# Performance work log

Hardware: AMD Instinct MI355X
Metric: run time of the kernel (lower is better)

## Reference

```python
import jax, jax.numpy as jnp
import numpy as np

B, D, H, T = 2048, 16, 256, 50
BETA_MIN, BETA_MAX = 0.1, 20.0


def setup_inputs() -> dict:
    key = jax.random.key(0)
    ks = jax.random.split(key, 6)
    s1 = 1.0 / np.sqrt(D)
    s2 = 1.0 / np.sqrt(H)
    return {
        "x": jax.random.normal(ks[0], (B, D), dtype=jnp.float32),
        "W1": jax.random.normal(ks[1], (D, H), dtype=jnp.float32) * s1,
        "b1": jnp.zeros((H,), dtype=jnp.float32),
        "wt": jax.random.normal(ks[2], (H,), dtype=jnp.float32) * 0.1,
        "W2": jax.random.normal(ks[3], (H, D), dtype=jnp.float32) * s2,
        "b2": jnp.zeros((D,), dtype=jnp.float32),
    }


def _dynamics(x, t, W1, b1, wt, W2, b2):
    # Reverse-time probability-flow ODE drift for a VP-SDE:
    #   dx/dt = f(x,t) - 0.5 * g(t)^2 * score(x,t)
    # with f = -0.5*beta(t)*x, g^2 = beta(t), score = MLP(x, t).
    beta = BETA_MIN + t * (BETA_MAX - BETA_MIN)
    h = jnp.tanh(x @ W1 + t * wt + b1)  # [B, H]
    score = h @ W2 + b2                 # [B, D]
    return -0.5 * beta * (x + score)


def _trace_jac(f, x):
    # Exact per-sample trace of the [D, D] Jacobian of f (batched over B)
    # via D forward-mode JVPs with basis tangents (batched, no per-output loop).
    eye = jnp.eye(x.shape[-1], dtype=x.dtype)

    def jvp_col(e):
        _, jv = jax.jvp(f, (x,), (jnp.broadcast_to(e, x.shape),))
        return jv  # [B, D]

    cols = jax.vmap(jvp_col)(eye)       # [D, B, D]
    return jnp.einsum("ibi->b", cols)   # sum of Jacobian diagonal per sample


def reference(x, W1, b1, wt, W2, b2):
    times = jnp.linspace(1e-3, 1.0, T, dtype=jnp.float32)

    def F(xc, t):
        dyn = lambda y: _dynamics(y, t, W1, b1, wt, W2, b2)
        dx = dyn(xc)
        tr = _trace_jac(dyn, xc)
        return dx, tr

    def rk4_step(carry, ts):
        xc, ldj = carry
        t0, t1 = ts
        h = t1 - t0
        k1x, k1t = F(xc, t0)
        k2x, k2t = F(xc + 0.5 * h * k1x, t0 + 0.5 * h)
        k3x, k3t = F(xc + 0.5 * h * k2x, t0 + 0.5 * h)
        k4x, k4t = F(xc + h * k3x, t1)
        xn = xc + (h / 6.0) * (k1x + 2.0 * k2x + 2.0 * k3x + k4x)
        ln = ldj + (h / 6.0) * (k1t + 2.0 * k2t + 2.0 * k3t + k4t)
        return (xn, ln), (xn, ln)

    ldj0 = jnp.zeros((x.shape[0],), dtype=x.dtype)
    (xf, ldjf), (xs, _) = jax.lax.scan(
        rk4_step, (x, ldj0), (times[:-1], times[1:])
    )
    xt = jnp.concatenate([x[None], xs], axis=0)  # [T, B, D] trajectory
    return xf, ldjf, xt
```

## Files before the change

### kernel.cpp

```cpp
#include <hip/hip_runtime.h>
#include <stdint.h>


typedef _Float16 f16x2 __attribute__((ext_vector_type(2)));

#if defined(__has_builtin)
#if __has_builtin(__builtin_amdgcn_fdot2)
#define HAVE_FDOT2 1
#endif
#endif

__device__ __forceinline__ float fdot2f(f16x2 a, f16x2 b, float c) {
#ifdef HAVE_FDOT2
    return __builtin_amdgcn_fdot2(a, b, c, false);
#else
    return fmaf((float)a.y, (float)b.y, fmaf((float)a.x, (float)b.x, c));
#endif
}

__device__ __forceinline__ uint32_t pkz(float a, float b) {
    auto v = __builtin_amdgcn_cvt_pkrtz(a, b);
    return __builtin_bit_cast(uint32_t, v);
}
__device__ __forceinline__ f16x2 upk(uint32_t u) {
    return __builtin_bit_cast(f16x2, u);
}

#define DPP_XOR1 0xB1
#define DPP_XOR2 0x4E
#define DPP_RHM  0x141
template <int CTRL>
__device__ __forceinline__ float dpp_add(float x) {
    int v = __builtin_amdgcn_update_dpp(
        0, __builtin_bit_cast(int, x), CTRL, 0xF, 0xF, true);
    return x + __builtin_bit_cast(float, v);
}

#define Bn 2048
#define Dn 16
#define Hn 256
#define Tn 50
#define CH 20

constexpr float T_LO = 1e-3f;
constexpr float DTc  = (1.0f - 1e-3f) / (float)(Tn - 1);
constexpr float W1W  = DTc * (1.f / 6.f);
constexpr float W2W  = DTc * (2.f / 6.f);

constexpr float nh_c(float t) { return -0.5f * (0.1f + 19.9f * t); }
constexpr float wbsum_c() {
    float s = 0.f;
    for (int j = 0; j < Tn - 1; ++j) {
        float t0 = T_LO + (float)j * DTc;
        float tm = t0 + 0.5f * DTc;
        float t1 = t0 + DTc;
        s += W1W * nh_c(t0) + 2.f * W2W * nh_c(tm) + W1W * nh_c(t1);
    }
    return s;
}
constexpr float WBSUM = wbsum_c();

__global__ __launch_bounds__(64) void ode_kernel(
    const float* __restrict__ x_in,
    const float* __restrict__ W1,
    const float* __restrict__ b1v,
    const float* __restrict__ wtv,
    const float* __restrict__ W2,
    const float* __restrict__ b2v,
    float* __restrict__ out)
{
    __shared__ __align__(16) uint32_t h_lds[8 * CH];

    const int L  = threadIdx.x;
    const int g8 = L >> 3;
    const int c  = L & 7;
    const int ia = 2 * g8, ib = ia + 1;
    const int k0 = 4 * L;
    const int gs = blockIdx.x;

    const float K2 = 2.88539008f;

    f16x2 w1p[4][8];
    float b1k[4], wtk[4], ck[4];
    #pragma unroll
    for (int q = 0; q < 4; ++q) {
        const int k = k0 + q;
        #pragma unroll
        for (int j = 0; j < 8; ++j) {
            f16x2 v;
            v.x = (_Float16)(K2 * W1[(2 * j)     * Hn + k]);
            v.y = (_Float16)(K2 * W1[(2 * j + 1) * Hn + k]);
            w1p[q][j] = v;
        }
        b1k[q] = K2 * b1v[k];
        wtk[q] = K2 * wtv[k];
        float s = 0.f;
        #pragma unroll
        for (int ii = 0; ii < 16; ++ii)
            s = fmaf(W1[ii * Hn + k], W2[k * Dn + ii], s);
        ck[q] = s;
    }
    const float cksum = (ck[0] + ck[1]) + (ck[2] + ck[3]);

    f16x2 w2a[16], w2b[16];
    #pragma unroll
    for (int m = 0; m < 16; ++m) {
        f16x2 va, vb;
        va.x = (_Float16)W2[(32 * c + 2 * m)     * Dn + ia];
        va.y = (_Float16)W2[(32 * c + 2 * m + 1) * Dn + ia];
        vb.x = (_Float16)W2[(32 * c + 2 * m)     * Dn + ib];
        vb.y = (_Float16)W2[(32 * c + 2 * m + 1) * Dn + ib];
        w2a[m] = va; w2b[m] = vb;
    }
    const float b2a8 = 0.125f * b2v[ia];
    const float b2b8 = 0.125f * b2v[ib];

    float xa = x_in[gs * Dn + ia];
    float xb = x_in[gs * Dn + ib];
    float ldjl = 0.f;

    float* xf_out  = out;
    float* ldj_out = out + (size_t)Bn * Dn;
    float* xt_ptr  = out + (size_t)Bn * Dn + Bn + gs * Dn + ia;

    if (c == 0) *(float2*)xt_ptr = make_float2(xa, xb);
    xt_ptr += Bn * Dn;

    const int hwidx = CH * (L >> 3) + 2 * (L & 7);

    uint32_t se0, se1, se2, se3, se4, se5, se6, se7;
    auto bcast = [&](float ea, float eb) {
        const uint32_t vpk = pkz(ea, eb);
        se0 = __builtin_amdgcn_readlane(vpk,  0);
        se1 = __builtin_amdgcn_readlane(vpk,  8);
        se2 = __builtin_amdgcn_readlane(vpk, 16);
        se3 = __builtin_amdgcn_readlane(vpk, 24);
        se4 = __builtin_amdgcn_readlane(vpk, 32);
        se5 = __builtin_amdgcn_readlane(vpk, 40);
        se6 = __builtin_amdgcn_readlane(vpk, 48);
        se7 = __builtin_amdgcn_readlane(vpk, 56);
    };

    auto Feval = [&](float xeva, float xevb, const float (&ui)[4],
                     float nhb, float wb, float& dxa, float& dxb) {
        const f16x2 xp[8] = { upk(se0), upk(se1), upk(se2), upk(se3),
                              upk(se4), upk(se5), upk(se6), upk(se7) };
        float u0 = ui[0], u1 = ui[1], u2 = ui[2], u3 = ui[3];
        #pragma unroll
        for (int j = 0; j < 8; ++j) {
            u0 = fdot2f(xp[j], w1p[0][j], u0);
            u1 = fdot2f(xp[j], w1p[1][j], u1);
            u2 = fdot2f(xp[j], w1p[2][j], u2);
            u3 = fdot2f(xp[j], w1p[3][j], u3);
        }
        const float h0 = fmaf(-2.f, __builtin_amdgcn_rcpf(__builtin_amdgcn_exp2f(u0) + 1.f), 1.f);
        const float h1 = fmaf(-2.f, __builtin_amdgcn_rcpf(__builtin_amdgcn_exp2f(u1) + 1.f), 1.f);
        const float h2 = fmaf(-2.f, __builtin_amdgcn_rcpf(__builtin_amdgcn_exp2f(u2) + 1.f), 1.f);
        const float h3 = fmaf(-2.f, __builtin_amdgcn_rcpf(__builtin_amdgcn_exp2f(u3) + 1.f), 1.f);
        *(uint2*)&h_lds[hwidx] = make_uint2(pkz(h0, h1), pkz(h2, h3));

        const float q0 = h0 * h0, q1 = h1 * h1, q2 = h2 * h2, q3 = h3 * h3;
        const float sq = fmaf(q0, ck[0], fmaf(q1, ck[1], fmaf(q2, ck[2], q3 * ck[3])));
        ldjl = fmaf(-wb, sq, ldjl);

        asm volatile("" ::: "memory");

        float sa0 = b2a8, sa1 = 0.f, sb0 = b2b8, sb1 = 0.f;
        #pragma unroll
        for (int mq = 0; mq < 4; ++mq) {
            const uint4 hv = *(const uint4*)&h_lds[CH * c + 4 * mq];
            const f16x2 p0 = upk(hv.x), p1 = upk(hv.y), p2 = upk(hv.z), p3 = upk(hv.w);
            sa0 = fdot2f(p0, w2a[4 * mq + 0], sa0);
            sb0 = fdot2f(p0, w2b[4 * mq + 0], sb0);
            sa1 = fdot2f(p1, w2a[4 * mq + 1], sa1);
            sb1 = fdot2f(p1, w2b[4 * mq + 1], sb1);
            sa0 = fdot2f(p2, w2a[4 * mq + 2], sa0);
            sb0 = fdot2f(p2, w2b[4 * mq + 2], sb0);
            sa1 = fdot2f(p3, w2a[4 * mq + 3], sa1);
            sb1 = fdot2f(p3, w2b[4 * mq + 3], sb1);
        }
        float sca = sa0 + sa1, scb = sb0 + sb1;
        sca = dpp_add<DPP_XOR1>(sca);  scb = dpp_add<DPP_XOR1>(scb);
        sca = dpp_add<DPP_XOR2>(sca);  scb = dpp_add<DPP_XOR2>(scb);
        sca = dpp_add<DPP_RHM >(sca);  scb = dpp_add<DPP_RHM >(scb);

        dxa = nhb * (xeva + sca);
        dxb = nhb * (xevb + scb);
    };

    float ui0[4], uim[4], uit[4];
    #pragma unroll
    for (int q = 0; q < 4; ++q) ui0[q] = fmaf(T_LO, wtk[q], b1k[q]);
    float nhb0 = -0.5f * fmaf(T_LO, 19.9f, 0.1f);

    bcast(xa, xb);
    for (int j = 0; j < Tn - 1; ++j) {
        const float t0 = fmaf((float)j, DTc, T_LO);
        const float tm = t0 + 0.5f * DTc;
        const float t1 = t0 + DTc;
        #pragma unroll
        for (int q = 0; q < 4; ++q) {
            uim[q] = fmaf(tm, wtk[q], b1k[q]);
            uit[q] = fmaf(t1, wtk[q], b1k[q]);
        }
        const float nhbm = -0.5f * fmaf(tm, 19.9f, 0.1f);
        const float nhb1 = -0.5f * fmaf(t1, 19.9f, 0.1f);
        const float wb0 = W1W * nhb0;
        const float wbm = W2W * nhbm;
        const float wb1 = W1W * nhb1;

        float k1a, k1b, k2a, k2b, k3a, k3b, k4a, k4b;

        Feval(xa, xb, ui0, nhb0, wb0, k1a, k1b);
        const float e2a = fmaf(0.5f * DTc, k1a, xa);
        const float e2b = fmaf(0.5f * DTc, k1b, xb);
        bcast(e2a, e2b);
        Feval(e2a, e2b, uim, nhbm, wbm, k2a, k2b);
        const float e3a = fmaf(0.5f * DTc, k2a, xa);
        const float e3b = fmaf(0.5f * DTc, k2b, xb);
        bcast(e3a, e3b);
        Feval(e3a, e3b, uim, nhbm, wbm, k3a, k3b);
        const float e4a = fmaf(DTc, k3a, xa);
        const float e4b = fmaf(DTc, k3b, xb);
        bcast(e4a, e4b);
        Feval(e4a, e4b, uit, nhb1, wb1, k4a, k4b);

        xa = fmaf(W1W, k1a + 2.f * (k2a + k3a) + k4a, xa);
        xb = fmaf(W1W, k1b + 2.f * (k2b + k3b) + k4b, xb);
        if (c == 0) *(float2*)xt_ptr = make_float2(xa, xb);
        xt_ptr += Bn * Dn;
        bcast(xa, xb);

        #pragma unroll
        for (int q = 0; q < 4; ++q) ui0[q] = uit[q];
        nhb0 = nhb1;
    }

    if (c == 0) *(float2*)(xf_out + gs * Dn + ia) = make_float2(xa, xb);

    ldjl = fmaf(cksum + 0.25f, WBSUM, ldjl);
    #pragma unroll
    for (int off = 1; off < 64; off <<= 1)
        ldjl += __shfl_xor(ldjl, off);
    if (L == 0) ldj_out[gs] = ldjl;
}

extern "C" void kernel_launch(void* const* d_in, const int* in_sizes, int n_in,
                              void* d_out, int out_size, void* d_ws, size_t ws_size,
                              hipStream_t stream) {
    const float* x  = (const float*)d_in[0];
    const float* W1 = (const float*)d_in[1];
    const float* b1 = (const float*)d_in[2];
    const float* wt = (const float*)d_in[3];
    const float* W2 = (const float*)d_in[4];
    const float* b2 = (const float*)d_in[5];
    (void)in_sizes; (void)n_in; (void)out_size; (void)d_ws; (void)ws_size;
    ode_kernel<<<Bn, 64, 0, stream>>>(x, W1, b1, wt, W2, b2, (float*)d_out);
}
```

Baseline: 171.9 us.

## Split hidden layer across two wavefronts per sample with double-buffered LDS

Each block now runs 128 threads (two wavefronts) per sample, and each thread handles 2 hidden units instead of 4. This halves the per-wave work in the first layer and the tanh. The second layer is redundantly computed by both waves from a shared, double-buffered LDS buffer of h, which now needs a block barrier on every function evaluation. The log-det partials from the two waves are combined through LDS at the end. The cost is 200 extra __syncthreads per sample, duplicated second-layer work, and more total waves in flight.

```diff
diff --git a/kernel.cpp b/kernel.cpp
--- a/kernel.cpp
+++ b/kernel.cpp
@@ -60,7 +60,7 @@
 }
 constexpr float WBSUM = wbsum_c();
 
-__global__ __launch_bounds__(64) void ode_kernel(
+__global__ __launch_bounds__(128) void ode_kernel(
     const float* __restrict__ x_in,
     const float* __restrict__ W1,
     const float* __restrict__ b1v,
@@ -69,22 +69,23 @@
     const float* __restrict__ b2v,
     float* __restrict__ out)
 {
-    __shared__ __align__(16) uint32_t h_lds[8 * CH];
-
-    const int L  = threadIdx.x;
-    const int g8 = L >> 3;
-    const int c  = L & 7;
+    __shared__ __align__(16) uint32_t h_lds[2][8 * CH];
+    __shared__ float ldj_x[2];
+
+    const int tid = threadIdx.x;
+    const int L   = tid & 63;
+    const int g8  = L >> 3;
+    const int c   = L & 7;
     const int ia = 2 * g8, ib = ia + 1;
-    const int k0 = 4 * L;
     const int gs = blockIdx.x;
 
     const float K2 = 2.88539008f;
 
-    f16x2 w1p[4][8];
-    float b1k[4], wtk[4], ck[4];
-    #pragma unroll
-    for (int q = 0; q < 4; ++q) {
-        const int k = k0 + q;
+    f16x2 w1p[2][8];
+    float b1k[2], wtk[2], ck[2];
+    #pragma unroll
+    for (int q = 0; q < 2; ++q) {
+        const int k = 2 * tid + q;
         #pragma unroll
         for (int j = 0; j < 8; ++j) {
             f16x2 v;
@@ -100,7 +101,7 @@
             s = fmaf(W1[ii * Hn + k], W2[k * Dn + ii], s);
         ck[q] = s;
     }
-    const float cksum = (ck[0] + ck[1]) + (ck[2] + ck[3]);
+    const float cks = ck[0] + ck[1];
 
     f16x2 w2a[16], w2b[16];
     #pragma unroll
@@ -123,10 +124,10 @@
     float* ldj_out = out + (size_t)Bn * Dn;
     float* xt_ptr  = out + (size_t)Bn * Dn + Bn + gs * Dn + ia;
 
-    if (c == 0) *(float2*)xt_ptr = make_float2(xa, xb);
+    if ((tid & 0x47) == 0) *(float2*)xt_ptr = make_float2(xa, xb);
     xt_ptr += Bn * Dn;
 
-    const int hwidx = CH * (L >> 3) + 2 * (L & 7);
+    const int hw = CH * (tid >> 4) + (tid & 15);
 
     uint32_t se0, se1, se2, se3, se4, se5, se6, se7;
     auto bcast = [&](float ea, float eb) {
@@ -141,34 +142,34 @@
         se7 = __builtin_amdgcn_readlane(vpk, 56);
     };
 
-    auto Feval = [&](float xeva, float xevb, const float (&ui)[4],
+    int fe = 0;
+
+    auto Feval = [&](float xeva, float xevb, const float (&ui)[2],
                      float nhb, float wb, float& dxa, float& dxb) {
+        uint32_t* hb = h_lds[fe & 1]; ++fe;
+
         const f16x2 xp[8] = { upk(se0), upk(se1), upk(se2), upk(se3),
                               upk(se4), upk(se5), upk(se6), upk(se7) };
-        float u0 = ui[0], u1 = ui[1], u2 = ui[2], u3 = ui[3];
+        float u0 = ui[0], u1 = ui[1];
         #pragma unroll
         for (int j = 0; j < 8; ++j) {
             u0 = fdot2f(xp[j], w1p[0][j], u0);
             u1 = fdot2f(xp[j], w1p[1][j], u1);
-            u2 = fdot2f(xp[j], w1p[2][j], u2);
-            u3 = fdot2f(xp[j], w1p[3][j], u3);
         }
         const float h0 = fmaf(-2.f, __builtin_amdgcn_rcpf(__builtin_amdgcn_exp2f(u0) + 1.f), 1.f);
         const float h1 = fmaf(-2.f, __builtin_amdgcn_rcpf(__builtin_amdgcn_exp2f(u1) + 1.f), 1.f);
-        const float h2 = fmaf(-2.f, __builtin_amdgcn_rcpf(__builtin_amdgcn_exp2f(u2) + 1.f), 1.f);
-        const float h3 = fmaf(-2.f, __builtin_amdgcn_rcpf(__builtin_amdgcn_exp2f(u3) + 1.f), 1.f);
-        *(uint2*)&h_lds[hwidx] = make_uint2(pkz(h0, h1), pkz(h2, h3));
-
-        const float q0 = h0 * h0, q1 = h1 * h1, q2 = h2 * h2, q3 = h3 * h3;
-        const float sq = fmaf(q0, ck[0], fmaf(q1, ck[1], fmaf(q2, ck[2], q3 * ck[3])));
+        hb[hw] = pkz(h0, h1);
+
+        const float q0 = h0 * h0, q1 = h1 * h1;
+        const float sq = fmaf(q0, ck[0], q1 * ck[1]);
         ldjl = fmaf(-wb, sq, ldjl);
 
-        asm volatile("" ::: "memory");
+        __syncthreads();
 
         float sa0 = b2a8, sa1 = 0.f, sb0 = b2b8, sb1 = 0.f;
         #pragma unroll
         for (int mq = 0; mq < 4; ++mq) {
-            const uint4 hv = *(const uint4*)&h_lds[CH * c + 4 * mq];
+            const uint4 hv = *(const uint4*)&hb[CH * c + 4 * mq];
             const f16x2 p0 = upk(hv.x), p1 = upk(hv.y), p2 = upk(hv.z), p3 = upk(hv.w);
             sa0 = fdot2f(p0, w2a[4 * mq + 0], sa0);
             sb0 = fdot2f(p0, w2b[4 * mq + 0], sb0);
@@ -188,9 +189,9 @@
         dxb = nhb * (xevb + scb);
     };
 
-    float ui0[4], uim[4], uit[4];
-    #pragma unroll
-    for (int q = 0; q < 4; ++q) ui0[q] = fmaf(T_LO, wtk[q], b1k[q]);
+    float ui0[2], uim[2], uit[2];
+    #pragma unroll
+    for (int q = 0; q < 2; ++q) ui0[q] = fmaf(T_LO, wtk[q], b1k[q]);
     float nhb0 = -0.5f * fmaf(T_LO, 19.9f, 0.1f);
 
     bcast(xa, xb);
@@ -199,7 +200,7 @@
         const float tm = t0 + 0.5f * DTc;
         const float t1 = t0 + DTc;
         #pragma unroll
-        for (int q = 0; q < 4; ++q) {
+        for (int q = 0; q < 2; ++q) {
             uim[q] = fmaf(tm, wtk[q], b1k[q]);
             uit[q] = fmaf(t1, wtk[q], b1k[q]);
         }
@@ -227,22 +228,24 @@
 
         xa = fmaf(W1W, k1a + 2.f * (k2a + k3a) + k4a, xa);
         xb = fmaf(W1W, k1b + 2.f * (k2b + k3b) + k4b, xb);
-        if (c == 0) *(float2*)xt_ptr = make_float2(xa, xb);
+        if ((tid & 0x47) == 0) *(float2*)xt_ptr = make_float2(xa, xb);
         xt_ptr += Bn * Dn;
         bcast(xa, xb);
 
         #pragma unroll
-        for (int q = 0; q < 4; ++q) ui0[q] = uit[q];
+        for (int q = 0; q < 2; ++q) ui0[q] = uit[q];
         nhb0 = nhb1;
     }
 
-    if (c == 0) *(float2*)(xf_out + gs * Dn + ia) = make_float2(xa, xb);
-
-    ldjl = fmaf(cksum + 0.25f, WBSUM, ldjl);
+    if ((tid & 0x47) == 0) *(float2*)(xf_out + gs * Dn + ia) = make_float2(xa, xb);
+
+    ldjl = fmaf(cks + 0.125f, WBSUM, ldjl);
     #pragma unroll
     for (int off = 1; off < 64; off <<= 1)
         ldjl += __shfl_xor(ldjl, off);
-    if (L == 0) ldj_out[gs] = ldjl;
+    if (L == 0) ldj_x[tid >> 6] = ldjl;
+    __syncthreads();
+    if (tid == 0) ldj_out[gs] = ldj_x[0] + ldj_x[1];
 }
 
 extern "C" void kernel_launch(void* const* d_in, const int* in_sizes, int n_in,
@@ -255,5 +258,5 @@
     const float* W2 = (const float*)d_in[4];
     const float* b2 = (const float*)d_in[5];
     (void)in_sizes; (void)n_in; (void)out_size; (void)d_ws; (void)ws_size;
-    ode_kernel<<<Bn, 64, 0, stream>>>(x, W1, b1, wt, W2, b2, (float*)d_out);
-}
+    ode_kernel<<<Bn, 128, 0, stream>>>(x, W1, b1, wt, W2, b2, (float*)d_out);
+}
```

Result: slower. 256.2 us (+49.1%).

## Process two batch samples per wavefront with interleaved RK4 evaluations

Applied to the files above, without the earlier changes.

Each 64-lane block now integrates two samples at once, interleaving their matvec dot products, tanh evaluations, LDS exchanges and DPP reductions, and the grid is halved. The aim is to raise instruction-level parallelism inside one wave so that the long serial dependency chains of each RK4 stage overlap, while weight registers and setup work are shared. The cost is fewer resident waves for latency hiding and higher register pressure.

```diff
diff --git a/kernel.cpp b/kernel.cpp
--- a/kernel.cpp
+++ b/kernel.cpp
@@ -69,14 +69,14 @@
     const float* __restrict__ b2v,
     float* __restrict__ out)
 {
-    __shared__ __align__(16) uint32_t h_lds[8 * CH];
+    __shared__ __align__(16) uint32_t h_lds[2][8 * CH];
 
     const int L  = threadIdx.x;
     const int g8 = L >> 3;
     const int c  = L & 7;
     const int ia = 2 * g8, ib = ia + 1;
     const int k0 = 4 * L;
-    const int gs = blockIdx.x;
+    const int gs0 = 2 * blockIdx.x, gs1 = gs0 + 1;
 
     const float K2 = 2.88539008f;
 
@@ -115,77 +115,111 @@
     const float b2a8 = 0.125f * b2v[ia];
     const float b2b8 = 0.125f * b2v[ib];
 
-    float xa = x_in[gs * Dn + ia];
-    float xb = x_in[gs * Dn + ib];
-    float ldjl = 0.f;
+    float xa0 = x_in[gs0 * Dn + ia], xb0 = x_in[gs0 * Dn + ib];
+    float xa1 = x_in[gs1 * Dn + ia], xb1 = x_in[gs1 * Dn + ib];
+    float ldj0 = 0.f, ldj1 = 0.f;
 
     float* xf_out  = out;
     float* ldj_out = out + (size_t)Bn * Dn;
-    float* xt_ptr  = out + (size_t)Bn * Dn + Bn + gs * Dn + ia;
-
-    if (c == 0) *(float2*)xt_ptr = make_float2(xa, xb);
+    float* xt_ptr  = out + (size_t)Bn * Dn + Bn + gs0 * Dn + ia;
+
+    if (c == 0) {
+        *(float2*)xt_ptr        = make_float2(xa0, xb0);
+        *(float2*)(xt_ptr + Dn) = make_float2(xa1, xb1);
+    }
     xt_ptr += Bn * Dn;
 
     const int hwidx = CH * (L >> 3) + 2 * (L & 7);
 
-    uint32_t se0, se1, se2, se3, se4, se5, se6, se7;
-    auto bcast = [&](float ea, float eb) {
+    uint32_t se[8], te[8];
+    auto bcast = [&](float ea, float eb, uint32_t (&sg)[8]) {
         const uint32_t vpk = pkz(ea, eb);
-        se0 = __builtin_amdgcn_readlane(vpk,  0);
-        se1 = __builtin_amdgcn_readlane(vpk,  8);
-        se2 = __builtin_amdgcn_readlane(vpk, 16);
-        se3 = __builtin_amdgcn_readlane(vpk, 24);
-        se4 = __builtin_amdgcn_readlane(vpk, 32);
-        se5 = __builtin_amdgcn_readlane(vpk, 40);
-        se6 = __builtin_amdgcn_readlane(vpk, 48);
-        se7 = __builtin_amdgcn_readlane(vpk, 56);
+        sg[0] = __builtin_amdgcn_readlane(vpk,  0);
+        sg[1] = __builtin_amdgcn_readlane(vpk,  8);
+        sg[2] = __builtin_amdgcn_readlane(vpk, 16);
+        sg[3] = __builtin_amdgcn_readlane(vpk, 24);
+        sg[4] = __builtin_amdgcn_readlane(vpk, 32);
+        sg[5] = __builtin_amdgcn_readlane(vpk, 40);
+        sg[6] = __builtin_amdgcn_readlane(vpk, 48);
+        sg[7] = __builtin_amdgcn_readlane(vpk, 56);
     };
 
-    auto Feval = [&](float xeva, float xevb, const float (&ui)[4],
-                     float nhb, float wb, float& dxa, float& dxb) {
-        const f16x2 xp[8] = { upk(se0), upk(se1), upk(se2), upk(se3),
-                              upk(se4), upk(se5), upk(se6), upk(se7) };
-        float u0 = ui[0], u1 = ui[1], u2 = ui[2], u3 = ui[3];
+    auto Feval = [&](float xva0, float xvb0, float xva1, float xvb1,
+                     const float (&ui)[4], float nhb, float wb,
+                     float& dxa0, float& dxb0, float& dxa1, float& dxb1) {
+        float u00 = ui[0], u01 = ui[1], u02 = ui[2], u03 = ui[3];
+        float u10 = ui[0], u11 = ui[1], u12 = ui[2], u13 = ui[3];
         #pragma unroll
         for (int j = 0; j < 8; ++j) {
-            u0 = fdot2f(xp[j], w1p[0][j], u0);
-            u1 = fdot2f(xp[j], w1p[1][j], u1);
-            u2 = fdot2f(xp[j], w1p[2][j], u2);
-            u3 = fdot2f(xp[j], w1p[3][j], u3);
-        }
-        const float h0 = fmaf(-2.f, __builtin_amdgcn_rcpf(__builtin_amdgcn_exp2f(u0) + 1.f), 1.f);
-        const float h1 = fmaf(-2.f, __builtin_amdgcn_rcpf(__builtin_amdgcn_exp2f(u1) + 1.f), 1.f);
-        const float h2 = fmaf(-2.f, __builtin_amdgcn_rcpf(__builtin_amdgcn_exp2f(u2) + 1.f), 1.f);
-        const float h3 = fmaf(-2.f, __builtin_amdgcn_rcpf(__builtin_amdgcn_exp2f(u3) + 1.f), 1.f);
-        *(uint2*)&h_lds[hwidx] = make_uint2(pkz(h0, h1), pkz(h2, h3));
-
-        const float q0 = h0 * h0, q1 = h1 * h1, q2 = h2 * h2, q3 = h3 * h3;
-        const float sq = fmaf(q0, ck[0], fmaf(q1, ck[1], fmaf(q2, ck[2], q3 * ck[3])));
-        ldjl = fmaf(-wb, sq, ldjl);
+            const f16x2 xp0 = upk(se[j]);
+            const f16x2 xp1 = upk(te[j]);
+            u00 = fdot2f(xp0, w1p[0][j], u00);
+            u10 = fdot2f(xp1, w1p[0][j], u10);
+            u01 = fdot2f(xp0, w1p[1][j], u01);
+            u11 = fdot2f(xp1, w1p[1][j], u11);
+            u02 = fdot2f(xp0, w1p[2][j], u02);
+            u12 = fdot2f(xp1, w1p[2][j], u12);
+            u03 = fdot2f(xp0, w1p[3][j], u03);
+            u13 = fdot2f(xp1, w1p[3][j], u13);
+        }
+        const float h00 = fmaf(-2.f, __builtin_amdgcn_rcpf(__builtin_amdgcn_exp2f(u00) + 1.f), 1.f);
+        const float h01 = fmaf(-2.f, __builtin_amdgcn_rcpf(__builtin_amdgcn_exp2f(u01) + 1.f), 1.f);
+        const float h02 = fmaf(-2.f, __builtin_amdgcn_rcpf(__builtin_amdgcn_exp2f(u02) + 1.f), 1.f);
+        const float h03 = fmaf(-2.f, __builtin_amdgcn_rcpf(__builtin_amdgcn_exp2f(u03) + 1.f), 1.f);
+        const float h10 = fmaf(-2.f, __builtin_amdgcn_rcpf(__builtin_amdgcn_exp2f(u10) + 1.f), 1.f);
+        const float h11 = fmaf(-2.f, __builtin_amdgcn_rcpf(__builtin_amdgcn_exp2f(u11) + 1.f), 1.f);
+        const float h12 = fmaf(-2.f, __builtin_amdgcn_rcpf(__builtin_amdgcn_exp2f(u12) + 1.f), 1.f);
+        const float h13 = fmaf(-2.f, __builtin_amdgcn_rcpf(__builtin_amdgcn_exp2f(u13) + 1.f), 1.f);
+        *(uint2*)&h_lds[0][hwidx] = make_uint2(pkz(h00, h01), pkz(h02, h03));
+        *(uint2*)&h_lds[1][hwidx] = make_uint2(pkz(h10, h11), pkz(h12, h13));
+
+        const float sq0 = fmaf(h00 * h00, ck[0], fmaf(h01 * h01, ck[1],
+                          fmaf(h02 * h02, ck[2], (h03 * h03) * ck[3])));
+        const float sq1 = fmaf(h10 * h10, ck[0], fmaf(h11 * h11, ck[1],
+                          fmaf(h12 * h12, ck[2], (h13 * h13) * ck[3])));
+        ldj0 = fmaf(-wb, sq0, ldj0);
+        ldj1 = fmaf(-wb, sq1, ldj1);
 
         asm volatile("" ::: "memory");
 
         float sa0 = b2a8, sa1 = 0.f, sb0 = b2b8, sb1 = 0.f;
+        float ra0 = b2a8, ra1 = 0.f, rb0 = b2b8, rb1 = 0.f;
         #pragma unroll
         for (int mq = 0; mq < 4; ++mq) {
-            const uint4 hv = *(const uint4*)&h_lds[CH * c + 4 * mq];
-            const f16x2 p0 = upk(hv.x), p1 = upk(hv.y), p2 = upk(hv.z), p3 = upk(hv.w);
-            sa0 = fdot2f(p0, w2a[4 * mq + 0], sa0);
-            sb0 = fdot2f(p0, w2b[4 * mq + 0], sb0);
-            sa1 = fdot2f(p1, w2a[4 * mq + 1], sa1);
-            sb1 = fdot2f(p1, w2b[4 * mq + 1], sb1);
-            sa0 = fdot2f(p2, w2a[4 * mq + 2], sa0);
-            sb0 = fdot2f(p2, w2b[4 * mq + 2], sb0);
-            sa1 = fdot2f(p3, w2a[4 * mq + 3], sa1);
-            sb1 = fdot2f(p3, w2b[4 * mq + 3], sb1);
-        }
-        float sca = sa0 + sa1, scb = sb0 + sb1;
-        sca = dpp_add<DPP_XOR1>(sca);  scb = dpp_add<DPP_XOR1>(scb);
-        sca = dpp_add<DPP_XOR2>(sca);  scb = dpp_add<DPP_XOR2>(scb);
-        sca = dpp_add<DPP_RHM >(sca);  scb = dpp_add<DPP_RHM >(scb);
-
-        dxa = nhb * (xeva + sca);
-        dxb = nhb * (xevb + scb);
+            const uint4 hv0 = *(const uint4*)&h_lds[0][CH * c + 4 * mq];
+            const uint4 hv1 = *(const uint4*)&h_lds[1][CH * c + 4 * mq];
+            const f16x2 p00 = upk(hv0.x), p01 = upk(hv0.y), p02 = upk(hv0.z), p03 = upk(hv0.w);
+            const f16x2 p10 = upk(hv1.x), p11 = upk(hv1.y), p12 = upk(hv1.z), p13 = upk(hv1.w);
+            sa0 = fdot2f(p00, w2a[4 * mq + 0], sa0);
+            ra0 = fdot2f(p10, w2a[4 * mq + 0], ra0);
+            sb0 = fdot2f(p00, w2b[4 * mq + 0], sb0);
+            rb0 = fdot2f(p10, w2b[4 * mq + 0], rb0);
+            sa1 = fdot2f(p01, w2a[4 * mq + 1], sa1);
+            ra1 = fdot2f(p11, w2a[4 * mq + 1], ra1);
+            sb1 = fdot2f(p01, w2b[4 * mq + 1], sb1);
+            rb1 = fdot2f(p11, w2b[4 * mq + 1], rb1);
+            sa0 = fdot2f(p02, w2a[4 * mq + 2], sa0);
+            ra0 = fdot2f(p12, w2a[4 * mq + 2], ra0);
+            sb0 = fdot2f(p02, w2b[4 * mq + 2], sb0);
+            rb0 = fdot2f(p12, w2b[4 * mq + 2], rb0);
+            sa1 = fdot2f(p03, w2a[4 * mq + 3], sa1);
+            ra1 = fdot2f(p13, w2a[4 * mq + 3], ra1);
+            sb1 = fdot2f(p03, w2b[4 * mq + 3], sb1);
+            rb1 = fdot2f(p13, w2b[4 * mq + 3], rb1);
+        }
+        float sca0 = sa0 + sa1, scb0 = sb0 + sb1;
+        float sca1 = ra0 + ra1, scb1 = rb0 + rb1;
+        sca0 = dpp_add<DPP_XOR1>(sca0);  scb0 = dpp_add<DPP_XOR1>(scb0);
+        sca1 = dpp_add<DPP_XOR1>(sca1);  scb1 = dpp_add<DPP_XOR1>(scb1);
+        sca0 = dpp_add<DPP_XOR2>(sca0);  scb0 = dpp_add<DPP_XOR2>(scb0);
+        sca1 = dpp_add<DPP_XOR2>(sca1);  scb1 = dpp_add<DPP_XOR2>(scb1);
+        sca0 = dpp_add<DPP_RHM >(sca0);  scb0 = dpp_add<DPP_RHM >(scb0);
+        sca1 = dpp_add<DPP_RHM >(sca1);  scb1 = dpp_add<DPP_RHM >(scb1);
+
+        dxa0 = nhb * (xva0 + sca0);
+        dxb0 = nhb * (xvb0 + scb0);
+        dxa1 = nhb * (xva1 + sca1);
+        dxb1 = nhb * (xvb1 + scb1);
     };
 
     float ui0[4], uim[4], uit[4];
@@ -193,7 +227,8 @@
     for (int q = 0; q < 4; ++q) ui0[q] = fmaf(T_LO, wtk[q], b1k[q]);
     float nhb0 = -0.5f * fmaf(T_LO, 19.9f, 0.1f);
 
-    bcast(xa, xb);
+    bcast(xa0, xb0, se);
+    bcast(xa1, xb1, te);
     for (int j = 0; j < Tn - 1; ++j) {
         const float t0 = fmaf((float)j, DTc, T_LO);
         const float tm = t0 + 0.5f * DTc;
@@ -209,40 +244,65 @@
         const float wbm = W2W * nhbm;
         const float wb1 = W1W * nhb1;
 
-        float k1a, k1b, k2a, k2b, k3a, k3b, k4a, k4b;
-
-        Feval(xa, xb, ui0, nhb0, wb0, k1a, k1b);
-        const float e2a = fmaf(0.5f * DTc, k1a, xa);
-        const float e2b = fmaf(0.5f * DTc, k1b, xb);
-        bcast(e2a, e2b);
-        Feval(e2a, e2b, uim, nhbm, wbm, k2a, k2b);
-        const float e3a = fmaf(0.5f * DTc, k2a, xa);
-        const float e3b = fmaf(0.5f * DTc, k2b, xb);
-        bcast(e3a, e3b);
-        Feval(e3a, e3b, uim, nhbm, wbm, k3a, k3b);
-        const float e4a = fmaf(DTc, k3a, xa);
-        const float e4b = fmaf(DTc, k3b, xb);
-        bcast(e4a, e4b);
-        Feval(e4a, e4b, uit, nhb1, wb1, k4a, k4b);
-
-        xa = fmaf(W1W, k1a + 2.f * (k2a + k3a) + k4a, xa);
-        xb = fmaf(W1W, k1b + 2.f * (k2b + k3b) + k4b, xb);
-        if (c == 0) *(float2*)xt_ptr = make_float2(xa, xb);
+        float k1a0, k1b0, k2a0, k2b0, k3a0, k3b0, k4a0, k4b0;
+        float k1a1, k1b1, k2a1, k2b1, k3a1, k3b1, k4a1, k4b1;
+
+        Feval(xa0, xb0, xa1, xb1, ui0, nhb0, wb0, k1a0, k1b0, k1a1, k1b1);
+        const float e2a0 = fmaf(0.5f * DTc, k1a0, xa0);
+        const float e2b0 = fmaf(0.5f * DTc, k1b0, xb0);
+        const float e2a1 = fmaf(0.5f * DTc, k1a1, xa1);
+        const float e2b1 = fmaf(0.5f * DTc, k1b1, xb1);
+        bcast(e2a0, e2b0, se);
+        bcast(e2a1, e2b1, te);
+        Feval(e2a0, e2b0, e2a1, e2b1, uim, nhbm, wbm, k2a0, k2b0, k2a1, k2b1);
+        const float e3a0 = fmaf(0.5f * DTc, k2a0, xa0);
+        const float e3b0 = fmaf(0.5f * DTc, k2b0, xb0);
+        const float e3a1 = fmaf(0.5f * DTc, k2a1, xa1);
+        const float e3b1 = fmaf(0.5f * DTc, k2b1, xb1);
+        bcast(e3a0, e3b0, se);
+        bcast(e3a1, e3b1, te);
+        Feval(e3a0, e3b0, e3a1, e3b1, uim, nhbm, wbm, k3a0, k3b0, k3a1, k3b1);
+        const float e4a0 = fmaf(DTc, k3a0, xa0);
+        const float e4b0 = fmaf(DTc, k3b0, xb0);
+        const float e4a1 = fmaf(DTc, k3a1, xa1);
+        const float e4b1 = fmaf(DTc, k3b1, xb1);
+        bcast(e4a0, e4b0, se);
+        bcast(e4a1, e4b1, te);
+        Feval(e4a0, e4b0, e4a1, e4b1, uit, nhb1, wb1, k4a0, k4b0, k4a1, k4b1);
+
+        xa0 = fmaf(W1W, k1a0 + 2.f * (k2a0 + k3a0) + k4a0, xa0);
+        xb0 = fmaf(W1W, k1b0 + 2.f * (k2b0 + k3b0) + k4b0, xb0);
+        xa1 = fmaf(W1W, k1a1 + 2.f * (k2a1 + k3a1) + k4a1, xa1);
+        xb1 = fmaf(W1W, k1b1 + 2.f * (k2b1 + k3b1) + k4b1, xb1);
+        if (c == 0) {
+            *(float2*)xt_ptr        = make_float2(xa0, xb0);
+            *(float2*)(xt_ptr + Dn) = make_float2(xa1, xb1);
+        }
         xt_ptr += Bn * Dn;
-        bcast(xa, xb);
+        bcast(xa0, xb0, se);
+        bcast(xa1, xb1, te);
 
         #pragma unroll
         for (int q = 0; q < 4; ++q) ui0[q] = uit[q];
         nhb0 = nhb1;
     }
 
-    if (c == 0) *(float2*)(xf_out + gs * Dn + ia) = make_float2(xa, xb);
-
-    ldjl = fmaf(cksum + 0.25f, WBSUM, ldjl);
+    if (c == 0) {
+        *(float2*)(xf_out + gs0 * Dn + ia) = make_float2(xa0, xb0);
+        *(float2*)(xf_out + gs1 * Dn + ia) = make_float2(xa1, xb1);
+    }
+
+    ldj0 = fmaf(cksum + 0.25f, WBSUM, ldj0);
+    ldj1 = fmaf(cksum + 0.25f, WBSUM, ldj1);
     #pragma unroll
-    for (int off = 1; off < 64; off <<= 1)
-        ldjl += __shfl_xor(ldjl, off);
-    if (L == 0) ldj_out[gs] = ldjl;
+    for (int off = 1; off < 64; off <<= 1) {
+        ldj0 += __shfl_xor(ldj0, off);
+        ldj1 += __shfl_xor(ldj1, off);
+    }
+    if (L == 0) {
+        ldj_out[gs0] = ldj0;
+        ldj_out[gs1] = ldj1;
+    }
 }
 
 extern "C" void kernel_launch(void* const* d_in, const int* in_sizes, int n_in,
@@ -255,5 +315,5 @@
     const float* W2 = (const float*)d_in[4];
     const float* b2 = (const float*)d_in[5];
     (void)in_sizes; (void)n_in; (void)out_size; (void)d_ws; (void)ws_size;
-    ode_kernel<<<Bn, 64, 0, stream>>>(x, W1, b1, wt, W2, b2, (float*)d_out);
-}
+    ode_kernel<<<Bn / 2, 64, 0, stream>>>(x, W1, b1, wt, W2, b2, (float*)d_out);
+}
```

Result: no change. 173.5 us (+1.0%).
